# Kernel tuning notes

Measured on AMD Instinct MI355X. Metric: run time of the kernel, lower is better.

## Reference

```python
import jax, jax.numpy as jnp
import numpy as np
import math

C, NH, HD, L, P, FFN = 256, 8, 32, 1, 4, 512
H_BEV, W_BEV = 200, 100
NQ, BS, NV = 1000, 4, H_BEV * W_BEV
EPS = 1e-5


def _ln(x, g, b):
    m = x.mean(-1, keepdims=True)
    v = ((x - m) ** 2).mean(-1, keepdims=True)
    return (x - m) / jnp.sqrt(v + EPS) * g + b


def _mha(x, qpos, in_w, in_b, ow, ob):
    # nn.MultiheadAttention self-attention; key_pos = query_pos (shapes match)
    q = x + qpos
    k = x + qpos
    v = x
    wq, wk, wv = jnp.split(in_w, 3, axis=0)
    bq, bk, bv = jnp.split(in_b, 3, axis=0)
    bs, nq, _ = x.shape
    qh = (q @ wq.T + bq).reshape(bs, nq, NH, HD)
    kh = (k @ wk.T + bk).reshape(bs, nq, NH, HD)
    vh = (v @ wv.T + bv).reshape(bs, nq, NH, HD)
    scores = jnp.einsum('bqhd,bkhd->bhqk', qh, kh) / jnp.sqrt(jnp.float32(HD))
    attn = jax.nn.softmax(scores, axis=-1)
    out = jnp.einsum('bhqk,bkhd->bqhd', attn, vh).reshape(bs, nq, C)
    return out @ ow.T + ob


def _msdeform(x, qpos, value, ref, spatial_shapes, so_w, so_b, aw_w, aw_b, vp_w, vp_b, op_w, op_b):
    # Multi-scale deformable attention (single level), bilinear sampling with
    # align_corners=False convention and zero padding, as in the CUDA kernel.
    bs, nq, _ = x.shape
    q = x + qpos
    v = (value @ vp_w.T + vp_b).reshape(bs, NV, NH, HD).transpose(0, 2, 1, 3)  # [bs,nh,nv,hd]
    off = (q @ so_w.T + so_b).reshape(bs, nq, NH, L, P, 2)
    aw = jax.nn.softmax((q @ aw_w.T + aw_b).reshape(bs, nq, NH, L * P), axis=-1)
    aw = aw.reshape(bs, nq, NH, L, P)
    norm = jnp.stack([spatial_shapes[:, 1], spatial_shapes[:, 0]], -1).astype(jnp.float32)  # [L,2] = (W,H)
    loc = ref[:, :, None, :, None, :] + off / norm[None, None, None, :, None, :]  # [bs,nq,nh,L,P,2]
    loc = loc[:, :, :, 0]  # single level -> [bs,nq,nh,P,2]
    awp = aw[:, :, :, 0]   # [bs,nq,nh,P]
    x_im = loc[..., 0] * W_BEV - 0.5
    y_im = loc[..., 1] * H_BEV - 0.5
    x0 = jnp.floor(x_im)
    y0 = jnp.floor(y_im)
    lx = x_im - x0
    ly = y_im - y0
    x0i = x0.astype(jnp.int32)
    y0i = y0.astype(jnp.int32)
    acc = jnp.zeros((bs, NH, nq, P, HD), jnp.float32)
    for dy in (0, 1):
        for dx in (0, 1):
            xi = x0i + dx
            yi = y0i + dy
            w = (lx if dx else 1.0 - lx) * (ly if dy else 1.0 - ly)  # [bs,nq,nh,P]
            ok = ((xi >= 0) & (xi < W_BEV) & (yi >= 0) & (yi < H_BEV)).astype(jnp.float32)
            idx = jnp.clip(yi, 0, H_BEV - 1) * W_BEV + jnp.clip(xi, 0, W_BEV - 1)
            idx_t = idx.transpose(0, 2, 1, 3).reshape(bs, NH, nq * P)
            g = jnp.take_along_axis(v, idx_t[..., None], axis=2).reshape(bs, NH, nq, P, HD)
            acc = acc + g * (w * ok).transpose(0, 2, 1, 3)[..., None]
    out = (acc * awp.transpose(0, 2, 1, 3)[..., None]).sum(3)  # [bs,nh,nq,hd]
    out = out.transpose(0, 2, 1, 3).reshape(bs, nq, C)
    return out @ op_w.T + op_b


def setup_inputs() -> dict:
    key = jax.random.key(0)
    ks = jax.random.split(key, 24)
    f32 = jnp.float32

    def w(k, shp):
        fan = shp[-1]
        return (jax.random.normal(k, shp, f32) * (1.0 / np.sqrt(fan))).astype(f32)

    # sampling_offsets bias per _reset_parameters (radial grid init)
    thetas = np.arange(NH, dtype=np.float32) * (2.0 * math.pi / NH)
    grid = np.stack([np.cos(thetas), np.sin(thetas)], -1)
    grid = grid / np.abs(grid).max(-1, keepdims=True)
    grid = np.tile(grid[:, None, None, :], (1, L, P, 1))
    for i in range(P):
        grid[:, :, i, :] *= i + 1
    so_b = jnp.asarray(grid.reshape(-1), f32)

    return {
        'query': jax.random.normal(ks[0], (NQ, BS, C), f32),
        'value': jax.random.normal(ks[1], (NV, BS, C), f32),
        'query_pos': jax.random.normal(ks[2], (NQ, BS, C), f32),
        'reference_points': jax.random.uniform(ks[3], (BS, NQ, L, 2), f32),
        'spatial_shapes': jnp.array([[H_BEV, W_BEV]], jnp.int32),
        'level_start_index': jnp.zeros((L,), jnp.int32),
        'in_proj_w': w(ks[4], (3 * C, C)),
        'in_proj_b': jnp.zeros((3 * C,), f32),
        'mha_ow': w(ks[5], (C, C)),
        'mha_ob': jnp.zeros((C,), f32),
        'so_w': w(ks[6], (NH * L * P * 2, C)) * 0.01,
        'so_b': so_b,
        'aw_w': w(ks[7], (NH * L * P, C)) * 0.01,
        'aw_b': jnp.zeros((NH * L * P,), f32),
        'vp_w': w(ks[8], (C, C)),
        'vp_b': jnp.zeros((C,), f32),
        'op_w': w(ks[9], (C, C)),
        'op_b': jnp.zeros((C,), f32),
        'ffn_w1': w(ks[10], (FFN, C)),
        'ffn_b1': jnp.zeros((FFN,), f32),
        'ffn_w2': w(ks[11], (C, FFN)),
        'ffn_b2': jnp.zeros((C,), f32),
        'ln1_g': jnp.ones((C,), f32), 'ln1_b': jnp.zeros((C,), f32),
        'ln2_g': jnp.ones((C,), f32), 'ln2_b': jnp.zeros((C,), f32),
        'ln3_g': jnp.ones((C,), f32), 'ln3_b': jnp.zeros((C,), f32),
    }


def reference(query, value, query_pos, reference_points, spatial_shapes, level_start_index,
              in_proj_w, in_proj_b, mha_ow, mha_ob, so_w, so_b, aw_w, aw_b,
              vp_w, vp_b, op_w, op_b, ffn_w1, ffn_b1, ffn_w2, ffn_b2,
              ln1_g, ln1_b, ln2_g, ln2_b, ln3_g, ln3_b):
    # batch_first=False: (seq, bs, C) -> (bs, seq, C)
    x = query.transpose(1, 0, 2)
    val = value.transpose(1, 0, 2)
    qpos = query_pos.transpose(1, 0, 2)
    # self_attn -> norm (residual inside attn wrapper; dropout=0 in eval)
    x = _ln(x + _mha(x, qpos, in_proj_w, in_proj_b, mha_ow, mha_ob), ln1_g, ln1_b)
    # cross_attn (MSDeformAttn) -> norm
    x = _ln(x + _msdeform(x, qpos, val, reference_points, spatial_shapes,
                          so_w, so_b, aw_w, aw_b, vp_w, vp_b, op_w, op_b), ln2_g, ln2_b)
    # ffn -> norm
    h = jax.nn.relu(x @ ffn_w1.T + ffn_b1) @ ffn_w2.T + ffn_b2
    x = _ln(x + h, ln3_g, ln3_b)
    return x.transpose(1, 0, 2)
```

## Files before the change

### kernel.cpp

```cpp
#include <hip/hip_runtime.h>
#include <hip/hip_bf16.h>
#include <cmath>

#define BS   4
#define NQ   1000
#define CDIM 256
#define NH   8
#define HD   32
#define NVAL 20000
#define FFND 512
#define PN   4
#define WBEV 100
#define HBEV 200
#define TK   64

typedef __bf16 v8bf __attribute__((ext_vector_type(8)));
typedef float  v4f  __attribute__((ext_vector_type(4)));

__device__ __forceinline__ void gload_lds16(const void* g, void* l) {
    __builtin_amdgcn_global_load_lds(
        (const __attribute__((address_space(1))) unsigned int*)g,
        (__attribute__((address_space(3))) unsigned int*)l, 16, 0, 0);
}

__device__ __forceinline__ void vgemm64_block(
    int vb, const float* __restrict__ value, const __bf16* __restrict__ Wv,
    const float* __restrict__ bv, __bf16* __restrict__ vpj, char* smem)
{
    __bf16* As = (__bf16*)smem;
    __bf16* Bs = (__bf16*)(smem + 8192);
    int tid = threadIdx.x;
    int wave = tid >> 6, lane = tid & 63, quad = lane >> 4, n16 = lane & 15;
    int bm = vb * 64;
    int wm = (wave & 1) * 32, wn = (wave >> 1) * 128;
    v4f acc[2][8] = {};

    for (int k0 = 0; k0 < 256; k0 += 64) {
        float4 fa[2][2];
        #pragma unroll
        for (int i = 0; i < 2; i++) {
            int e = i * 256 + tid;
            int r = e >> 3, c = (e & 7) ^ (r & 7);
            const float* p = value + (long)(bm + r) * 256 + k0 + c * 8;
            fa[i][0] = *(const float4*)p;
            fa[i][1] = *(const float4*)(p + 4);
        }
        __syncthreads();
        #pragma unroll
        for (int i = 0; i < 2; i++) {
            int e = i * 256 + tid;
            v8bf v;
            v[0] = (__bf16)fa[i][0].x; v[1] = (__bf16)fa[i][0].y;
            v[2] = (__bf16)fa[i][0].z; v[3] = (__bf16)fa[i][0].w;
            v[4] = (__bf16)fa[i][1].x; v[5] = (__bf16)fa[i][1].y;
            v[6] = (__bf16)fa[i][1].z; v[7] = (__bf16)fa[i][1].w;
            *(v8bf*)(As + e * 8) = v;
        }
        #pragma unroll
        for (int i = 0; i < 8; i++) {
            int e = i * 256 + tid;
            int r = e >> 3, c = (e & 7) ^ (r & 7);
            gload_lds16(Wv + (long)r * 256 + k0 + c * 8, Bs + e * 8);
        }
        __syncthreads();
        #pragma unroll
        for (int s = 0; s < 2; s++) {
            v8bf af[2], bfr[8];
            #pragma unroll
            for (int mi = 0; mi < 2; mi++) {
                int row = wm + mi * 16 + n16;
                af[mi] = *(v8bf*)&As[row * 64 + (((quad + s * 4) ^ (row & 7))) * 8];
            }
            #pragma unroll
            for (int nj = 0; nj < 8; nj++) {
                int row = wn + nj * 16 + n16;
                bfr[nj] = *(v8bf*)&Bs[row * 64 + (((quad + s * 4) ^ (row & 7))) * 8];
            }
            #pragma unroll
            for (int mi = 0; mi < 2; mi++)
                #pragma unroll
                for (int nj = 0; nj < 8; nj++)
                    acc[mi][nj] = __builtin_amdgcn_mfma_f32_16x16x32_bf16(af[mi], bfr[nj], acc[mi][nj], 0, 0, 0);
        }
    }
    #pragma unroll
    for (int mi = 0; mi < 2; mi++) {
        #pragma unroll
        for (int r = 0; r < 4; r++) {
            int m = bm + wm + mi * 16 + quad * 4 + r;
            #pragma unroll
            for (int nj = 0; nj < 8; nj++) {
                int nn = wn + nj * 16 + n16;
                vpj[(long)m * 256 + nn] = (__bf16)(acc[mi][nj][r] + bv[nn]);
            }
        }
    }
}

__global__ __launch_bounds__(256) void prep_all_kernel(
    const float* __restrict__ query, const float* __restrict__ qpos,
    const float* __restrict__ in_w, const float* __restrict__ mha_ow,
    const float* __restrict__ vp_w, const float* __restrict__ op_w,
    const float* __restrict__ ffn_w1, const float* __restrict__ ffn_w2,
    const float* __restrict__ so_w, const float* __restrict__ aw_w,
    const float* __restrict__ so_b, const float* __restrict__ aw_b,
    float* __restrict__ x, float* __restrict__ qpos_t,
    __bf16* __restrict__ x_bf, __bf16* __restrict__ xq_bf,
    __bf16* __restrict__ wb, __bf16* __restrict__ wsmall,
    float* __restrict__ bsmall)
{
    int blk = blockIdx.x, tid = threadIdx.x;
    if (blk < 640) {
        long e = ((long)blk * 256 + tid) * 4;
        const float* src; long off;
        if      (e < 196608) { src = in_w;   off = e; }
        else if (e < 262144) { src = mha_ow; off = e - 196608; }
        else if (e < 327680) { src = vp_w;   off = e - 262144; }
        else if (e < 393216) { src = op_w;   off = e - 327680; }
        else if (e < 524288) { src = ffn_w1; off = e - 393216; }
        else                 { src = ffn_w2; off = e - 524288; }
        float4 v = *(const float4*)(src + off);
        __bf16* d = wb + e;
        d[0] = (__bf16)v.x; d[1] = (__bf16)v.y; d[2] = (__bf16)v.z; d[3] = (__bf16)v.w;
    } else if (blk < 4640) {
        int qb = blk - 640;
        int q = qb / BS, b = qb % BS;
        float qv = query[(q * BS + b) * CDIM + tid];
        float pv = qpos [(q * BS + b) * CDIM + tid];
        int o = (b * NQ + q) * CDIM + tid;
        x[o] = qv; qpos_t[o] = pv;
        x_bf[o] = (__bf16)qv; xq_bf[o] = (__bf16)(qv + pv);
    } else if (blk < 4672) {
        long e = ((long)(blk - 4640) * 256 + tid) * 4;
        int row = (int)(e >> 8), col = (int)(e & 255);
        float4 v = {0.f, 0.f, 0.f, 0.f};
        if (row < 64)      v = *(const float4*)(so_w + row * 256 + col);
        else if (row < 96) v = *(const float4*)(aw_w + (row - 64) * 256 + col);
        __bf16* d = wsmall + e;
        d[0] = (__bf16)v.x; d[1] = (__bf16)v.y; d[2] = (__bf16)v.z; d[3] = (__bf16)v.w;
    } else {
        if (tid < 128) bsmall[tid] = tid < 64 ? so_b[tid] : (tid < 96 ? aw_b[tid - 64] : 0.f);
    }
}

__global__ __launch_bounds__(256) void qkvv_kernel(
    const __bf16* __restrict__ xq, const __bf16* __restrict__ xv,
    const __bf16* __restrict__ W, const float* __restrict__ bias,
    __bf16* __restrict__ qk, __bf16* __restrict__ vh,
    const float* __restrict__ value, const __bf16* __restrict__ Wv,
    const float* __restrict__ bv, __bf16* __restrict__ vpj, int voff)
{
    __shared__ __align__(16) char smem[40960];
    int tid = threadIdx.x;
    if ((int)blockIdx.x >= 756) {
        vgemm64_block(blockIdx.x - 756 + voff, value, Wv, bv, vpj, smem);
        return;
    }
    int blk = blockIdx.x;
    int bn = (blk % 12) * 64, bm = (blk / 12) * 64;
    __bf16* As = (__bf16*)smem;
    __bf16* Bs = (__bf16*)(smem + 8192);
    const __bf16* A = (bn < 512) ? xq : xv;
    int wave = tid >> 6, lane = tid & 63, quad = lane >> 4, n16 = lane & 15;
    int wm = (wave & 1) * 32, wn = (wave >> 1) * 32;
    v4f acc[2][2] = {};

    for (int k0 = 0; k0 < 256; k0 += 64) {
        __syncthreads();
        #pragma unroll
        for (int i = 0; i < 2; i++) {
            int e = i * 256 + tid;
            int r = e >> 3, c = (e & 7) ^ (r & 7);
            int row = bm + r; if (row > BS * NQ - 1) row = BS * NQ - 1;
            gload_lds16(A + (long)row * 256 + k0 + c * 8, As + e * 8);
        }
        #pragma unroll
        for (int i = 0; i < 2; i++) {
            int e = i * 256 + tid;
            int r = e >> 3, c = (e & 7) ^ (r & 7);
            gload_lds16(W + (long)(bn + r) * 256 + k0 + c * 8, Bs + e * 8);
        }
        __syncthreads();
        #pragma unroll
        for (int s = 0; s < 2; s++) {
            v8bf af[2], bfr[2];
            #pragma unroll
            for (int mi = 0; mi < 2; mi++) {
                int row = wm + mi * 16 + n16;
                af[mi] = *(v8bf*)&As[row * 64 + (((quad + s * 4) ^ (row & 7))) * 8];
            }
            #pragma unroll
            for (int nj = 0; nj < 2; nj++) {
                int row = wn + nj * 16 + n16;
                bfr[nj] = *(v8bf*)&Bs[row * 64 + (((quad + s * 4) ^ (row & 7))) * 8];
            }
            #pragma unroll
            for (int mi = 0; mi < 2; mi++)
                #pragma unroll
                for (int nj = 0; nj < 2; nj++)
                    acc[mi][nj] = __builtin_amdgcn_mfma_f32_16x16x32_bf16(af[mi], bfr[nj], acc[mi][nj], 0, 0, 0);
        }
    }

    #pragma unroll
    for (int mi = 0; mi < 2; mi++) {
        #pragma unroll
        for (int r = 0; r < 4; r++) {
            int m = bm + wm + mi * 16 + quad * 4 + r;
            if (m >= BS * NQ) continue;
            #pragma unroll
            for (int nj = 0; nj < 2; nj++) {
                int nn = bn + wn + nj * 16 + n16;
                float v = acc[mi][nj][r] + bias[nn];
                if (nn < 512) qk[(long)m * 512 + nn] = (__bf16)v;
                else          vh[(long)m * 256 + (nn - 512)] = (__bf16)v;
            }
        }
    }
}

__global__ __launch_bounds__(256) void fattnv_kernel(
    const __bf16* __restrict__ qk, const __bf16* __restrict__ vh,
    __bf16* __restrict__ aout,
    const float* __restrict__ value, const __bf16* __restrict__ Wv,
    const float* __restrict__ bv, __bf16* __restrict__ vpj, int voff)
{
    __shared__ __align__(16) char smem[40960];
    int tid = threadIdx.x;
    if ((int)blockIdx.x >= 512) {
        vgemm64_block(blockIdx.x - 512 + voff, value, Wv, bv, vpj, smem);
        return;
    }
    int fb = blockIdx.x;
    int qt = fb & 15, h = (fb >> 4) & 7, b = fb >> 7;
    __bf16* Ks = (__bf16*)smem;
    __bf16* Vt = (__bf16*)(smem + 10240);
    __bf16* Pl = (__bf16*)(smem + 19456);
    int wave = tid >> 6, lane = tid & 63, quad = lane >> 4, n = lane & 15;
    int q0 = qt * 64 + wave * 16;
    const float scale = 0.17677669529663687f;
    const float M0 = 8.0f;

    int qrow = q0 + n; if (qrow > NQ - 1) qrow = NQ - 1;
    v8bf aq = *(const v8bf*)(qk + (long)(b * NQ + qrow) * 512 + h * HD + quad * 8);

    v4f o0 = {}, o1 = {};
    float lp[4] = {0.f, 0.f, 0.f, 0.f};

    int sv = tid >> 7;
    int t2 = tid & 127;
    int key = t2 & 63;
    int d16 = (t2 >> 6) * 16;

    v8bf stg0, stg1;
    auto loadtile = [&](int k0) {
        int krow = k0 + key; if (krow > NQ - 1) krow = NQ - 1;
        const __bf16* p = sv ? (vh + (long)(b * NQ + krow) * CDIM + h * HD + d16)
                             : (qk + (long)(b * NQ + krow) * 512 + 256 + h * HD + d16);
        stg0 = *(const v8bf*)p;
        stg1 = *(const v8bf*)(p + 8);
    };

    loadtile(0);
    int pb = 0;
    for (int k0 = 0; k0 < NQ; k0 += TK) {
        if (sv == 0) {
            *(v8bf*)&Ks[(pb * 64 + key) * 40 + d16]     = stg0;
            *(v8bf*)&Ks[(pb * 64 + key) * 40 + d16 + 8] = stg1;
        } else {
            #pragma unroll
            for (int j = 0; j < 8; j++) {
                Vt[(pb * 32 + d16 + j) * 72 + key]            = stg0[j];
                Vt[(pb * 32 + d16 + 8 + j) * 72 + (key ^ 16)] = stg1[j];
            }
        }
        if (k0 + TK < NQ) loadtile(k0 + TK);
        __syncthreads();

        v8bf bk0 = *(v8bf*)&Ks[(pb * 64 +      n) * 40 + quad * 8];
        v8bf bk1 = *(v8bf*)&Ks[(pb * 64 + 16 + n) * 40 + quad * 8];
        v8bf bk2 = *(v8bf*)&Ks[(pb * 64 + 32 + n) * 40 + quad * 8];
        v8bf bk3 = *(v8bf*)&Ks[(pb * 64 + 48 + n) * 40 + quad * 8];
        v4f z = {};
        v4f S0 = __builtin_amdgcn_mfma_f32_16x16x32_bf16(aq, bk0, z, 0, 0, 0);
        v4f S1 = __builtin_amdgcn_mfma_f32_16x16x32_bf16(aq, bk1, z, 0, 0, 0);
        v4f S2 = __builtin_amdgcn_mfma_f32_16x16x32_bf16(aq, bk2, z, 0, 0, 0);
        v4f S3 = __builtin_amdgcn_mfma_f32_16x16x32_bf16(aq, bk3, z, 0, 0, 0);

        bool last = (k0 + TK > NQ);
        float p0[4], p1[4], p2[4], p3[4];
        #pragma unroll
        for (int r = 0; r < 4; r++) {
            p0[r] = __expf(fmaf(S0[r], scale, -M0));
            p1[r] = __expf(fmaf(S1[r], scale, -M0));
            p2[r] = __expf(fmaf(S2[r], scale, -M0));
            p3[r] = __expf(fmaf(S3[r], scale, -M0));
            if (last) {
                if (k0 + 32 + n >= NQ) p2[r] = 0.f;
                if (k0 + 48 + n >= NQ) p3[r] = 0.f;
            }
            lp[r] += p0[r] + p1[r] + p2[r] + p3[r];
        }
        #pragma unroll
        for (int r = 0; r < 4; r++) {
            __bf16* pp = &Pl[(wave * 16 + quad * 4 + r) * 72];
            pp[n]      = (__bf16)p0[r];
            pp[16 + n] = (__bf16)p1[r];
            pp[32 + n] = (__bf16)p2[r];
            pp[48 + n] = (__bf16)p3[r];
        }
        asm volatile("s_waitcnt lgkmcnt(0)" ::: "memory");
        v8bf ap0 = *(v8bf*)&Pl[(wave * 16 + n) * 72 + quad * 8];
        v8bf ap1 = *(v8bf*)&Pl[(wave * 16 + n) * 72 + 32 + quad * 8];
        int swz = ((n >> 3) & 1) << 4;
        int c0 = (quad * 8) ^ swz;
        int c1 = (32 + quad * 8) ^ swz;
        v8bf bv00 = *(v8bf*)&Vt[(pb * 32 +      n) * 72 + c0];
        v8bf bv01 = *(v8bf*)&Vt[(pb * 32 +      n) * 72 + c1];
        v8bf bv10 = *(v8bf*)&Vt[(pb * 32 + 16 + n) * 72 + c0];
        v8bf bv11 = *(v8bf*)&Vt[(pb * 32 + 16 + n) * 72 + c1];
        o0 = __builtin_amdgcn_mfma_f32_16x16x32_bf16(ap0, bv00, o0, 0, 0, 0);
        o0 = __builtin_amdgcn_mfma_f32_16x16x32_bf16(ap1, bv01, o0, 0, 0, 0);
        o1 = __builtin_amdgcn_mfma_f32_16x16x32_bf16(ap0, bv10, o1, 0, 0, 0);
        o1 = __builtin_amdgcn_mfma_f32_16x16x32_bf16(ap1, bv11, o1, 0, 0, 0);
        pb ^= 1;
    }

    #pragma unroll
    for (int r = 0; r < 4; r++) {
        float l = lp[r];
        #pragma unroll
        for (int off = 1; off < 16; off <<= 1) l += __shfl_xor(l, off, 16);
        int q = q0 + quad * 4 + r;
        if (q < NQ) {
            float invl = 1.0f / l;
            __bf16* op = aout + ((long)(b * NQ + q) * CDIM + h * HD);
            op[n]      = (__bf16)(o0[r] * invl);
            op[16 + n] = (__bf16)(o1[r] * invl);
        }
    }
}

__global__ __launch_bounds__(256) void gln1s_kernel(
    const __bf16* __restrict__ A, const __bf16* __restrict__ W,
    const float* __restrict__ bias, const float* __restrict__ res,
    const float* __restrict__ g, const float* __restrict__ beta,
    const float* __restrict__ qpos_t,
    const __bf16* __restrict__ Wsm, const float* __restrict__ bsm,
    float* __restrict__ outf, float* __restrict__ soawO,
    const float* __restrict__ value, const __bf16* __restrict__ Wv,
    const float* __restrict__ bv, __bf16* __restrict__ vpj, int voff)
{
    __shared__ __align__(16) char smem[43776];
    int tid = threadIdx.x;
    if ((int)blockIdx.x >= 250) {
        vgemm64_block(blockIdx.x - 250 + voff, value, Wv, bv, vpj, smem);
        return;
    }
    __bf16* As  = (__bf16*)smem;
    __bf16* Bs  = (__bf16*)(smem + 2048);
    __bf16* Axq = (__bf16*)(smem + 34816);
    float* redS = (float*)(smem + 43264);
    float* redQ = redS + 64;
    int bm = blockIdx.x * 16;
    int wave = tid >> 6, lane = tid & 63, quad = lane >> 4, n16 = lane & 15;
    int wn = wave * 64;
    v4f acc[4] = {};

    for (int k0 = 0; k0 < 256; k0 += 64) {
        __syncthreads();
        if (tid < 128) {
            int e = tid;
            int r = e >> 3, c = (e & 7) ^ (r & 7);
            gload_lds16(A + (long)(bm + r) * 256 + k0 + c * 8, As + e * 8);
        }
        #pragma unroll
        for (int i = 0; i < 8; i++) {
            int e = i * 256 + tid;
            int r = e >> 3, c = (e & 7) ^ (r & 7);
            gload_lds16(W + (long)r * 256 + k0 + c * 8, Bs + e * 8);
        }
        __syncthreads();
        #pragma unroll
        for (int s = 0; s < 2; s++) {
            v8bf af = *(v8bf*)&As[n16 * 64 + (((quad + s * 4) ^ (n16 & 7))) * 8];
            #pragma unroll
            for (int nj = 0; nj < 4; nj++) {
                int row = wn + nj * 16 + n16;
                v8bf bfr = *(v8bf*)&Bs[row * 64 + (((quad + s * 4) ^ (row & 7))) * 8];
                acc[nj] = __builtin_amdgcn_mfma_f32_16x16x32_bf16(af, bfr, acc[nj], 0, 0, 0);
            }
        }
    }

    float y[4][4], s1[4] = {}, s2[4] = {};
    #pragma unroll
    for (int r = 0; r < 4; r++) {
        int m = bm + quad * 4 + r;
        #pragma unroll
        for (int nj = 0; nj < 4; nj++) {
            int nn = wn + nj * 16 + n16;
            float v = acc[nj][r] + bias[nn] + res[(long)m * 256 + nn];
            y[r][nj] = v;
            s1[r] += v; s2[r] += v * v;
        }
    }
    #pragma unroll
    for (int r = 0; r < 4; r++) {
        #pragma unroll
        for (int off = 1; off < 16; off <<= 1) {
            s1[r] += __shfl_xor(s1[r], off, 16);
            s2[r] += __shfl_xor(s2[r], off, 16);
        }
    }
    if (n16 == 0) {
        #pragma unroll
        for (int r = 0; r < 4; r++) {
            redS[wave * 16 + quad * 4 + r] = s1[r];
            redQ[wave * 16 + quad * 4 + r] = s2[r];
        }
    }
    __syncthreads();
    #pragma unroll
    for (int r = 0; r < 4; r++) {
        int mr = quad * 4 + r;
        float ts = redS[mr] + redS[16 + mr] + redS[32 + mr] + redS[48 + mr];
        float tq = redQ[mr] + redQ[16 + mr] + redQ[32 + mr] + redQ[48 + mr];
        float mean = ts * (1.0f / 256.0f);
        float var = tq * (1.0f / 256.0f) - mean * mean;
        float rinv = rsqrtf(var + 1e-5f);
        int m = bm + mr;
        #pragma unroll
        for (int nj = 0; nj < 4; nj++) {
            int nn = wn + nj * 16 + n16;
            float o = (y[r][nj] - mean) * rinv * g[nn] + beta[nn];
            outf[(long)m * 256 + nn] = o;
            Axq[mr * 264 + nn] = (__bf16)(o + qpos_t[(long)m * 256 + nn]);
        }
    }
    __syncthreads();
    if (wave < 3) {
        v4f sacc[2] = {};
        #pragma unroll
        for (int k0 = 0; k0 < 256; k0 += 32) {
            v8bf af = *(v8bf*)&Axq[n16 * 264 + k0 + quad * 8];
            #pragma unroll
            for (int t = 0; t < 2; t++) {
                int col = wave * 32 + t * 16 + n16;
                v8bf bw = *(const v8bf*)(Wsm + (long)col * 256 + k0 + quad * 8);
                sacc[t] = __builtin_amdgcn_mfma_f32_16x16x32_bf16(af, bw, sacc[t], 0, 0, 0);
            }
        }
        #pragma unroll
        for (int t = 0; t < 2; t++)
            #pragma unroll
            for (int r = 0; r < 4; r++) {
                int mm = bm + quad * 4 + r;
                int col = wave * 32 + t * 16 + n16;
                soawO[(long)mm * 96 + col] = sacc[t][r] + bsm[col];
            }
    }
}

__global__ __launch_bounds__(256) void msds_kernel(
    const __bf16* __restrict__ vproj, const float* __restrict__ soaw,
    const float* __restrict__ refp, __bf16* __restrict__ out)
{
    int bq = blockIdx.x; int b = bq / NQ; int q = bq % NQ;
    int t = threadIdx.x; int h = t / HD; int d = t % HD;
    float rx = refp[(b * NQ + q) * 2 + 0];
    float ry = refp[(b * NQ + q) * 2 + 1];
    const float* rowp = soaw + (long)(b * NQ + q) * 96;
    const float* offp = rowp + h * 8;
    const float* awp  = rowp + 64 + h * 4;
    float a0 = awp[0], a1 = awp[1], a2 = awp[2], a3 = awp[3];
    float m = fmaxf(fmaxf(a0, a1), fmaxf(a2, a3));
    float e0 = __expf(a0 - m), e1 = __expf(a1 - m), e2 = __expf(a2 - m), e3 = __expf(a3 - m);
    float invs = 1.0f / (e0 + e1 + e2 + e3);
    float acc = 0.f;
    #pragma unroll
    for (int p = 0; p < PN; p++) {
        float ew = (p == 0 ? e0 : p == 1 ? e1 : p == 2 ? e2 : e3) * invs;
        float xim = rx * (float)WBEV + offp[p * 2 + 0] - 0.5f;
        float yim = ry * (float)HBEV + offp[p * 2 + 1] - 0.5f;
        float x0f = floorf(xim), y0f = floorf(yim);
        float lx = xim - x0f, ly = yim - y0f;
        int x0 = (int)x0f, y0 = (int)y0f;
        float gsum = 0.f;
        #pragma unroll
        for (int dy = 0; dy < 2; dy++) {
            #pragma unroll
            for (int dx = 0; dx < 2; dx++) {
                int xi = x0 + dx, yi = y0 + dy;
                float w = (dx ? lx : 1.f - lx) * (dy ? ly : 1.f - ly);
                bool ok = (xi >= 0 && xi < WBEV && yi >= 0 && yi < HBEV);
                int xc = min(max(xi, 0), WBEV - 1);
                int yc = min(max(yi, 0), HBEV - 1);
                int idx = yc * WBEV + xc;
                float gv = (float)vproj[((long)(idx * BS + b)) * CDIM + h * HD + d];
                gsum += (ok ? w : 0.f) * gv;
            }
        }
        acc += ew * gsum;
    }
    out[(b * NQ + q) * CDIM + h * HD + d] = (__bf16)acc;
}

__global__ __launch_bounds__(256) void gln2_kernel(
    const __bf16* __restrict__ A, const __bf16* __restrict__ W,
    const float* __restrict__ bias, const float* __restrict__ res,
    const float* __restrict__ g, const float* __restrict__ beta,
    float* __restrict__ outf, __bf16* __restrict__ outb)
{
    __shared__ __align__(16) char smem[35328];
    __bf16* As = (__bf16*)smem;
    __bf16* Bs = (__bf16*)(smem + 2048);
    float* redS = (float*)(smem + 34816);
    float* redQ = redS + 64;
    int tid = threadIdx.x;
    int bm = blockIdx.x * 16;
    int wave = tid >> 6, lane = tid & 63, quad = lane >> 4, n16 = lane & 15;
    int wn = wave * 64;
    v4f acc[4] = {};

    for (int k0 = 0; k0 < 256; k0 += 64) {
        __syncthreads();
        if (tid < 128) {
            int e = tid;
            int r = e >> 3, c = (e & 7) ^ (r & 7);
            gload_lds16(A + (long)(bm + r) * 256 + k0 + c * 8, As + e * 8);
        }
        #pragma unroll
        for (int i = 0; i < 8; i++) {
            int e = i * 256 + tid;
            int r = e >> 3, c = (e & 7) ^ (r & 7);
            gload_lds16(W + (long)r * 256 + k0 + c * 8, Bs + e * 8);
        }
        __syncthreads();
        #pragma unroll
        for (int s = 0; s < 2; s++) {
            v8bf af = *(v8bf*)&As[n16 * 64 + (((quad + s * 4) ^ (n16 & 7))) * 8];
            #pragma unroll
            for (int nj = 0; nj < 4; nj++) {
                int row = wn + nj * 16 + n16;
                v8bf bfr = *(v8bf*)&Bs[row * 64 + (((quad + s * 4) ^ (row & 7))) * 8];
                acc[nj] = __builtin_amdgcn_mfma_f32_16x16x32_bf16(af, bfr, acc[nj], 0, 0, 0);
            }
        }
    }

    float y[4][4], s1[4] = {}, s2[4] = {};
    #pragma unroll
    for (int r = 0; r < 4; r++) {
        int m = bm + quad * 4 + r;
        #pragma unroll
        for (int nj = 0; nj < 4; nj++) {
            int nn = wn + nj * 16 + n16;
            float v = acc[nj][r] + bias[nn] + res[(long)m * 256 + nn];
            y[r][nj] = v;
            s1[r] += v; s2[r] += v * v;
        }
    }
    #pragma unroll
    for (int r = 0; r < 4; r++) {
        #pragma unroll
        for (int off = 1; off < 16; off <<= 1) {
            s1[r] += __shfl_xor(s1[r], off, 16);
            s2[r] += __shfl_xor(s2[r], off, 16);
        }
    }
    if (n16 == 0) {
        #pragma unroll
        for (int r = 0; r < 4; r++) {
            redS[wave * 16 + quad * 4 + r] = s1[r];
            redQ[wave * 16 + quad * 4 + r] = s2[r];
        }
    }
    __syncthreads();
    #pragma unroll
    for (int r = 0; r < 4; r++) {
        int mr = quad * 4 + r;
        float ts = redS[mr] + redS[16 + mr] + redS[32 + mr] + redS[48 + mr];
        float tq = redQ[mr] + redQ[16 + mr] + redQ[32 + mr] + redQ[48 + mr];
        float mean = ts * (1.0f / 256.0f);
        float var = tq * (1.0f / 256.0f) - mean * mean;
        float rinv = rsqrtf(var + 1e-5f);
        int m = bm + mr;
        #pragma unroll
        for (int nj = 0; nj < 4; nj++) {
            int nn = wn + nj * 16 + n16;
            float o = (y[r][nj] - mean) * rinv * g[nn] + beta[nn];
            outf[(long)m * 256 + nn] = o;
            outb[(long)m * 256 + nn] = (__bf16)o;
        }
    }
}

template<int TBM, int TBN>
__global__ __launch_bounds__(256) void mgemm_kernel(
    const __bf16* __restrict__ A, const __bf16* __restrict__ W,
    const float* __restrict__ bias, __bf16* __restrict__ Yb,
    int M, int N, int K, int relu, int nx)
{
    constexpr int SZ = TBM * 128 + TBN * 128;
    __shared__ __align__(16) char smem[SZ];
    constexpr int WMF = TBM / 32;
    constexpr int WNF = TBN / 32;
    __bf16* As = (__bf16*)smem;
    __bf16* Bs = (__bf16*)(smem + TBM * 128);
    int bm = (blockIdx.x / nx) * TBM, bn = (blockIdx.x % nx) * TBN;
    int tid = threadIdx.x;
    int wave = tid >> 6, lane = tid & 63, quad = lane >> 4, n16 = lane & 15;
    int wm = (wave & 1) * (TBM / 2), wn = (wave >> 1) * (TBN / 2);
    v4f acc[WMF][WNF] = {};

    for (int k0 = 0; k0 < K; k0 += 64) {
        __syncthreads();
        #pragma unroll
        for (int i = 0; i < TBM * 8 / 256; i++) {
            int e = i * 256 + tid;
            int r = e >> 3, c = (e & 7) ^ (r & 7);
            int row = bm + r; if (row > M - 1) row = M - 1;
            gload_lds16(A + (long)row * K + k0 + c * 8, As + e * 8);
        }
        #pragma unroll
        for (int i = 0; i < TBN * 8 / 256; i++) {
            int e = i * 256 + tid;
            int r = e >> 3, c = (e & 7) ^ (r & 7);
            gload_lds16(W + (long)(bn + r) * K + k0 + c * 8, Bs + e * 8);
        }
        __syncthreads();
        #pragma unroll
        for (int s = 0; s < 2; s++) {
            v8bf af[WMF], bfr[WNF];
            #pragma unroll
            for (int mi = 0; mi < WMF; mi++) {
                int row = wm + mi * 16 + n16;
                af[mi] = *(v8bf*)&As[row * 64 + (((quad + s * 4) ^ (row & 7))) * 8];
            }
            #pragma unroll
            for (int nj = 0; nj < WNF; nj++) {
                int row = wn + nj * 16 + n16;
                bfr[nj] = *(v8bf*)&Bs[row * 64 + (((quad + s * 4) ^ (row & 7))) * 8];
            }
            #pragma unroll
            for (int mi = 0; mi < WMF; mi++)
                #pragma unroll
                for (int nj = 0; nj < WNF; nj++)
                    acc[mi][nj] = __builtin_amdgcn_mfma_f32_16x16x32_bf16(af[mi], bfr[nj], acc[mi][nj], 0, 0, 0);
        }
    }

    #pragma unroll
    for (int mi = 0; mi < WMF; mi++) {
        #pragma unroll
        for (int r = 0; r < 4; r++) {
            int m = bm + wm + mi * 16 + quad * 4 + r;
            if (m >= M) continue;
            #pragma unroll
            for (int nj = 0; nj < WNF; nj++) {
                int nn = bn + wn + nj * 16 + n16;
                if (nn >= N) continue;
                float v = acc[mi][nj][r] + bias[nn];
                if (relu) v = fmaxf(v, 0.f);
                Yb[(long)m * N + nn] = (__bf16)v;
            }
        }
    }
}

__global__ __launch_bounds__(256) void gln3_kernel(
    const __bf16* __restrict__ A, const __bf16* __restrict__ W,
    const float* __restrict__ bias, const float* __restrict__ res,
    const float* __restrict__ g, const float* __restrict__ beta,
    float* __restrict__ outf)
{
    __shared__ __align__(16) char smem[35328];
    __bf16* As = (__bf16*)smem;
    __bf16* Bs = (__bf16*)(smem + 2048);
    float* redS = (float*)(smem + 34816);
    float* redQ = redS + 64;
    int tid = threadIdx.x;
    int bm = blockIdx.x * 16;
    int wave = tid >> 6, lane = tid & 63, quad = lane >> 4, n16 = lane & 15;
    int wn = wave * 64;
    v4f acc[4] = {};

    for (int k0 = 0; k0 < 512; k0 += 64) {
        __syncthreads();
        if (tid < 128) {
            int e = tid;
            int r = e >> 3, c = (e & 7) ^ (r & 7);
            gload_lds16(A + (long)(bm + r) * 512 + k0 + c * 8, As + e * 8);
        }
        #pragma unroll
        for (int i = 0; i < 8; i++) {
            int e = i * 256 + tid;
            int r = e >> 3, c = (e & 7) ^ (r & 7);
            gload_lds16(W + (long)r * 512 + k0 + c * 8, Bs + e * 8);
        }
        __syncthreads();
        #pragma unroll
        for (int s = 0; s < 2; s++) {
            v8bf af = *(v8bf*)&As[n16 * 64 + (((quad + s * 4) ^ (n16 & 7))) * 8];
            #pragma unroll
            for (int nj = 0; nj < 4; nj++) {
                int row = wn + nj * 16 + n16;
                v8bf bfr = *(v8bf*)&Bs[row * 64 + (((quad + s * 4) ^ (row & 7))) * 8];
                acc[nj] = __builtin_amdgcn_mfma_f32_16x16x32_bf16(af, bfr, acc[nj], 0, 0, 0);
            }
        }
    }

    float y[4][4], s1[4] = {}, s2[4] = {};
    #pragma unroll
    for (int r = 0; r < 4; r++) {
        int m = bm + quad * 4 + r;
        #pragma unroll
        for (int nj = 0; nj < 4; nj++) {
            int nn = wn + nj * 16 + n16;
            float v = acc[nj][r] + bias[nn] + res[(long)m * 256 + nn];
            y[r][nj] = v;
            s1[r] += v; s2[r] += v * v;
        }
    }
    #pragma unroll
    for (int r = 0; r < 4; r++) {
        #pragma unroll
        for (int off = 1; off < 16; off <<= 1) {
            s1[r] += __shfl_xor(s1[r], off, 16);
            s2[r] += __shfl_xor(s2[r], off, 16);
        }
    }
    if (n16 == 0) {
        #pragma unroll
        for (int r = 0; r < 4; r++) {
            redS[wave * 16 + quad * 4 + r] = s1[r];
            redQ[wave * 16 + quad * 4 + r] = s2[r];
        }
    }
    __syncthreads();
    #pragma unroll
    for (int r = 0; r < 4; r++) {
        int mr = quad * 4 + r;
        float ts = redS[mr] + redS[16 + mr] + redS[32 + mr] + redS[48 + mr];
        float tq = redQ[mr] + redQ[16 + mr] + redQ[32 + mr] + redQ[48 + mr];
        float mean = ts * (1.0f / 256.0f);
        float var = tq * (1.0f / 256.0f) - mean * mean;
        float rinv = rsqrtf(var + 1e-5f);
        int m = bm + mr;
        int b = m / NQ, q = m - b * NQ;
        #pragma unroll
        for (int nj = 0; nj < 4; nj++) {
            int nn = wn + nj * 16 + n16;
            float o = (y[r][nj] - mean) * rinv * g[nn] + beta[nn];
            outf[(long)(q * BS + b) * 256 + nn] = o;
        }
    }
}

extern "C" void kernel_launch(void* const* d_in, const int* in_sizes, int n_in,
                              void* d_out, int out_size, void* d_ws, size_t ws_size,
                              hipStream_t stream) {
    const float* query = (const float*)d_in[0];
    const float* value = (const float*)d_in[1];
    const float* qpos  = (const float*)d_in[2];
    const float* refp  = (const float*)d_in[3];
    const float* in_w  = (const float*)d_in[6];
    const float* in_b  = (const float*)d_in[7];
    const float* mha_ow = (const float*)d_in[8];
    const float* mha_ob = (const float*)d_in[9];
    const float* so_w  = (const float*)d_in[10];
    const float* so_b  = (const float*)d_in[11];
    const float* aw_w  = (const float*)d_in[12];
    const float* aw_b  = (const float*)d_in[13];
    const float* vp_w  = (const float*)d_in[14];
    const float* vp_b  = (const float*)d_in[15];
    const float* op_w  = (const float*)d_in[16];
    const float* op_b  = (const float*)d_in[17];
    const float* ffn_w1 = (const float*)d_in[18];
    const float* ffn_b1 = (const float*)d_in[19];
    const float* ffn_w2 = (const float*)d_in[20];
    const float* ffn_b2 = (const float*)d_in[21];
    const float* ln1_g = (const float*)d_in[22];
    const float* ln1_b = (const float*)d_in[23];
    const float* ln2_g = (const float*)d_in[24];
    const float* ln2_b = (const float*)d_in[25];
    const float* ln3_g = (const float*)d_in[26];
    const float* ln3_b = (const float*)d_in[27];
    float* out = (float*)d_out;

    const long NTOK = (long)BS * NQ * CDIM;

    float* x      = (float*)d_ws;
    float* qpos_t = x + NTOK;
    float* x1     = qpos_t + NTOK;
    float* x2     = x1 + NTOK;
    float* soaw   = x2 + NTOK;
    float* bsmall = soaw + (long)BS * NQ * 96;
    __bf16* x_bf   = (__bf16*)(bsmall + 128);
    __bf16* xq_bf  = x_bf + NTOK;
    __bf16* qk_bf  = xq_bf + NTOK;
    __bf16* vh_bf  = qk_bf + 2 * NTOK;
    __bf16* aA_bf  = vh_bf + NTOK;
    __bf16* x2_bf  = aA_bf + NTOK;
    __bf16* h1_bf  = x2_bf + NTOK;
    __bf16* vpj_bf = h1_bf + 2 * NTOK;
    __bf16* wb     = vpj_bf + (long)BS * NVAL * CDIM;
    __bf16* inw_b  = wb;
    __bf16* mow_b  = wb + 196608;
    __bf16* vpw_b  = wb + 262144;
    __bf16* opw_b  = wb + 327680;
    __bf16* fw1_b  = wb + 393216;
    __bf16* fw2_b  = wb + 524288;
    __bf16* wsmall = wb + 655360;

    dim3 blk(256);

    prep_all_kernel<<<4673, blk, 0, stream>>>(
        query, qpos, in_w, mha_ow, vp_w, op_w, ffn_w1, ffn_w2,
        so_w, aw_w, so_b, aw_b,
        x, qpos_t, x_bf, xq_bf, wb, wsmall, bsmall);

    qkvv_kernel<<<1173, blk, 0, stream>>>(xq_bf, x_bf, inw_b, in_b, qk_bf, vh_bf,
                                          value, vpw_b, vp_b, vpj_bf, 0);

    fattnv_kernel<<<929, blk, 0, stream>>>(qk_bf, vh_bf, aA_bf,
                                           value, vpw_b, vp_b, vpj_bf, 417);

    gln1s_kernel<<<666, blk, 0, stream>>>(
        aA_bf, mow_b, mha_ob, x, ln1_g, ln1_b, qpos_t, wsmall, bsmall,
        x1, soaw, value, vpw_b, vp_b, vpj_bf, 834);

    msds_kernel<<<BS * NQ, blk, 0, stream>>>(vpj_bf, soaw, refp, aA_bf);

    gln2_kernel<<<250, blk, 0, stream>>>(
        aA_bf, opw_b, op_b, x1, ln2_g, ln2_b, x2, x2_bf);

    mgemm_kernel<64, 64><<<504, blk, 0, stream>>>(
        x2_bf, fw1_b, ffn_b1, h1_bf, BS * NQ, 512, 256, 1, 8);

    gln3_kernel<<<250, blk, 0, stream>>>(
        h1_bf, fw2_b, ffn_b2, x2, ln3_g, ln3_b, out);
}
```

Measured before the change: 274.9 us.

## Fuse output-proj/LN2, FFN and LN3 into one tail kernel; vectorize deformable sampling

Merges three kernels (out-proj with LN2, the FFN first GEMM, and the FFN second GEMM with LN3) into one per-16-row kernel. The LN2 output and the ReLU hidden activations stay in swizzled LDS, so the x2 and h1 intermediates are never written to or read from global memory. This removes two launches. The deformable sampling kernel now handles two queries per block and two channels per thread using bf16x2 loads. The cost is that the fused kernel runs only 250 blocks with larger LDS use, which lowers parallelism for the FFN GEMMs.

```diff
diff --git a/kernel.cpp b/kernel.cpp
--- a/kernel.cpp
+++ b/kernel.cpp
@@ -15,6 +15,7 @@
 #define TK   64
 
 typedef __bf16 v8bf __attribute__((ext_vector_type(8)));
+typedef __bf16 v2bf __attribute__((ext_vector_type(2)));
 typedef float  v4f  __attribute__((ext_vector_type(4)));
 
 __device__ __forceinline__ void gload_lds16(const void* g, void* l) {
@@ -466,8 +467,12 @@
     const __bf16* __restrict__ vproj, const float* __restrict__ soaw,
     const float* __restrict__ refp, __bf16* __restrict__ out)
 {
-    int bq = blockIdx.x; int b = bq / NQ; int q = bq % NQ;
-    int t = threadIdx.x; int h = t / HD; int d = t % HD;
+    int t = threadIdx.x;
+    int bq = blockIdx.x * 2 + (t >> 7);
+    int b = bq / NQ; int q = bq % NQ;
+    int t2 = t & 127;
+    int h = t2 >> 4;
+    int d0 = (t2 & 15) * 2;
     float rx = refp[(b * NQ + q) * 2 + 0];
     float ry = refp[(b * NQ + q) * 2 + 1];
     const float* rowp = soaw + (long)(b * NQ + q) * 96;
@@ -477,7 +482,7 @@
     float m = fmaxf(fmaxf(a0, a1), fmaxf(a2, a3));
     float e0 = __expf(a0 - m), e1 = __expf(a1 - m), e2 = __expf(a2 - m), e3 = __expf(a3 - m);
     float invs = 1.0f / (e0 + e1 + e2 + e3);
-    float acc = 0.f;
+    float accA = 0.f, accB = 0.f;
     #pragma unroll
     for (int p = 0; p < PN; p++) {
         float ew = (p == 0 ? e0 : p == 1 ? e1 : p == 2 ? e2 : e3) * invs;
@@ -486,7 +491,7 @@
         float x0f = floorf(xim), y0f = floorf(yim);
         float lx = xim - x0f, ly = yim - y0f;
         int x0 = (int)x0f, y0 = (int)y0f;
-        float gsum = 0.f;
+        float gA = 0.f, gB = 0.f;
         #pragma unroll
         for (int dy = 0; dy < 2; dy++) {
             #pragma unroll
@@ -497,32 +502,41 @@
                 int xc = min(max(xi, 0), WBEV - 1);
                 int yc = min(max(yi, 0), HBEV - 1);
                 int idx = yc * WBEV + xc;
-                float gv = (float)vproj[((long)(idx * BS + b)) * CDIM + h * HD + d];
-                gsum += (ok ? w : 0.f) * gv;
-            }
-        }
-        acc += ew * gsum;
-    }
-    out[(b * NQ + q) * CDIM + h * HD + d] = (__bf16)acc;
-}
-
-__global__ __launch_bounds__(256) void gln2_kernel(
-    const __bf16* __restrict__ A, const __bf16* __restrict__ W,
-    const float* __restrict__ bias, const float* __restrict__ res,
-    const float* __restrict__ g, const float* __restrict__ beta,
-    float* __restrict__ outf, __bf16* __restrict__ outb)
+                v2bf gv = *(const v2bf*)(vproj + ((long)(idx * BS + b)) * CDIM + h * HD + d0);
+                float wk = (ok ? w : 0.f);
+                gA += wk * (float)gv[0];
+                gB += wk * (float)gv[1];
+            }
+        }
+        accA += ew * gA;
+        accB += ew * gB;
+    }
+    v2bf o2; o2[0] = (__bf16)accA; o2[1] = (__bf16)accB;
+    *(v2bf*)(out + (long)(b * NQ + q) * CDIM + h * HD + d0) = o2;
+}
+
+__global__ __launch_bounds__(256) void gtail_kernel(
+    const __bf16* __restrict__ A, const __bf16* __restrict__ Wop,
+    const float* __restrict__ opb, const float* __restrict__ res,
+    const float* __restrict__ g2, const float* __restrict__ b2ln,
+    const __bf16* __restrict__ W1, const float* __restrict__ b1,
+    const __bf16* __restrict__ W2, const float* __restrict__ bff2,
+    const float* __restrict__ g3, const float* __restrict__ b3ln,
+    float* __restrict__ outf)
 {
-    __shared__ __align__(16) char smem[35328];
-    __bf16* As = (__bf16*)smem;
-    __bf16* Bs = (__bf16*)(smem + 2048);
-    float* redS = (float*)(smem + 34816);
-    float* redQ = redS + 64;
+    __shared__ __align__(16) char smem[59904];
+    __bf16* As  = (__bf16*)smem;
+    __bf16* Bs  = (__bf16*)(smem + 2048);
+    __bf16* As2 = (__bf16*)(smem + 34816);
+    __bf16* h1s = (__bf16*)(smem + 43008);
+    float* redS = (float*)(smem + 59392);
+    float* redQ = (float*)(smem + 59648);
     int tid = threadIdx.x;
     int bm = blockIdx.x * 16;
     int wave = tid >> 6, lane = tid & 63, quad = lane >> 4, n16 = lane & 15;
     int wn = wave * 64;
+
     v4f acc[4] = {};
-
     for (int k0 = 0; k0 < 256; k0 += 64) {
         __syncthreads();
         if (tid < 128) {
@@ -534,7 +548,7 @@
         for (int i = 0; i < 8; i++) {
             int e = i * 256 + tid;
             int r = e >> 3, c = (e & 7) ^ (r & 7);
-            gload_lds16(W + (long)r * 256 + k0 + c * 8, Bs + e * 8);
+            gload_lds16(Wop + (long)r * 256 + k0 + c * 8, Bs + e * 8);
         }
         __syncthreads();
         #pragma unroll
@@ -548,16 +562,15 @@
             }
         }
     }
-
-    float y[4][4], s1[4] = {}, s2[4] = {};
+    float yv[4][4], s1[4] = {}, s2[4] = {};
     #pragma unroll
     for (int r = 0; r < 4; r++) {
         int m = bm + quad * 4 + r;
         #pragma unroll
         for (int nj = 0; nj < 4; nj++) {
             int nn = wn + nj * 16 + n16;
-            float v = acc[nj][r] + bias[nn] + res[(long)m * 256 + nn];
-            y[r][nj] = v;
+            float v = acc[nj][r] + opb[nn] + res[(long)m * 256 + nn];
+            yv[r][nj] = v;
             s1[r] += v; s2[r] += v * v;
         }
     }
@@ -585,158 +598,101 @@
         float mean = ts * (1.0f / 256.0f);
         float var = tq * (1.0f / 256.0f) - mean * mean;
         float rinv = rsqrtf(var + 1e-5f);
-        int m = bm + mr;
         #pragma unroll
         for (int nj = 0; nj < 4; nj++) {
             int nn = wn + nj * 16 + n16;
-            float o = (y[r][nj] - mean) * rinv * g[nn] + beta[nn];
-            outf[(long)m * 256 + nn] = o;
-            outb[(long)m * 256 + nn] = (__bf16)o;
-        }
-    }
-}
-
-template<int TBM, int TBN>
-__global__ __launch_bounds__(256) void mgemm_kernel(
-    const __bf16* __restrict__ A, const __bf16* __restrict__ W,
-    const float* __restrict__ bias, __bf16* __restrict__ Yb,
-    int M, int N, int K, int relu, int nx)
-{
-    constexpr int SZ = TBM * 128 + TBN * 128;
-    __shared__ __align__(16) char smem[SZ];
-    constexpr int WMF = TBM / 32;
-    constexpr int WNF = TBN / 32;
-    __bf16* As = (__bf16*)smem;
-    __bf16* Bs = (__bf16*)(smem + TBM * 128);
-    int bm = (blockIdx.x / nx) * TBM, bn = (blockIdx.x % nx) * TBN;
-    int tid = threadIdx.x;
-    int wave = tid >> 6, lane = tid & 63, quad = lane >> 4, n16 = lane & 15;
-    int wm = (wave & 1) * (TBM / 2), wn = (wave >> 1) * (TBN / 2);
-    v4f acc[WMF][WNF] = {};
-
-    for (int k0 = 0; k0 < K; k0 += 64) {
-        __syncthreads();
-        #pragma unroll
-        for (int i = 0; i < TBM * 8 / 256; i++) {
-            int e = i * 256 + tid;
-            int r = e >> 3, c = (e & 7) ^ (r & 7);
-            int row = bm + r; if (row > M - 1) row = M - 1;
-            gload_lds16(A + (long)row * K + k0 + c * 8, As + e * 8);
-        }
-        #pragma unroll
-        for (int i = 0; i < TBN * 8 / 256; i++) {
-            int e = i * 256 + tid;
-            int r = e >> 3, c = (e & 7) ^ (r & 7);
-            gload_lds16(W + (long)(bn + r) * K + k0 + c * 8, Bs + e * 8);
-        }
-        __syncthreads();
-        #pragma unroll
-        for (int s = 0; s < 2; s++) {
-            v8bf af[WMF], bfr[WNF];
-            #pragma unroll
-            for (int mi = 0; mi < WMF; mi++) {
-                int row = wm + mi * 16 + n16;
-                af[mi] = *(v8bf*)&As[row * 64 + (((quad + s * 4) ^ (row & 7))) * 8];
-            }
-            #pragma unroll
-            for (int nj = 0; nj < WNF; nj++) {
-                int row = wn + nj * 16 + n16;
-                bfr[nj] = *(v8bf*)&Bs[row * 64 + (((quad + s * 4) ^ (row & 7))) * 8];
-            }
-            #pragma unroll
-            for (int mi = 0; mi < WMF; mi++)
+            float o = (yv[r][nj] - mean) * rinv * g2[nn] + b2ln[nn];
+            yv[r][nj] = o;
+            int c = nn & 63;
+            As2[wave * 1024 + mr * 64 + ((((c >> 3)) ^ (mr & 7)) << 3) + (c & 7)] = (__bf16)o;
+        }
+    }
+
+    #pragma unroll 1
+    for (int H = 0; H < 2; H++) {
+        v4f accB[4] = {};
+        for (int k0 = 0; k0 < 256; k0 += 64) {
+            __syncthreads();
+            #pragma unroll
+            for (int i = 0; i < 8; i++) {
+                int e = i * 256 + tid;
+                int r = e >> 3, c = (e & 7) ^ (r & 7);
+                gload_lds16(W1 + (long)(H * 256 + r) * 256 + k0 + c * 8, Bs + e * 8);
+            }
+            __syncthreads();
+            int kc = k0 >> 6;
+            #pragma unroll
+            for (int s = 0; s < 2; s++) {
+                v8bf af = *(v8bf*)&As2[kc * 1024 + n16 * 64 + (((quad + s * 4) ^ (n16 & 7))) * 8];
                 #pragma unroll
-                for (int nj = 0; nj < WNF; nj++)
-                    acc[mi][nj] = __builtin_amdgcn_mfma_f32_16x16x32_bf16(af[mi], bfr[nj], acc[mi][nj], 0, 0, 0);
-        }
-    }
-
-    #pragma unroll
-    for (int mi = 0; mi < WMF; mi++) {
+                for (int nj = 0; nj < 4; nj++) {
+                    int row = wn + nj * 16 + n16;
+                    v8bf bfr = *(v8bf*)&Bs[row * 64 + (((quad + s * 4) ^ (row & 7))) * 8];
+                    accB[nj] = __builtin_amdgcn_mfma_f32_16x16x32_bf16(af, bfr, accB[nj], 0, 0, 0);
+                }
+            }
+        }
         #pragma unroll
         for (int r = 0; r < 4; r++) {
-            int m = bm + wm + mi * 16 + quad * 4 + r;
-            if (m >= M) continue;
-            #pragma unroll
-            for (int nj = 0; nj < WNF; nj++) {
-                int nn = bn + wn + nj * 16 + n16;
-                if (nn >= N) continue;
-                float v = acc[mi][nj][r] + bias[nn];
-                if (relu) v = fmaxf(v, 0.f);
-                Yb[(long)m * N + nn] = (__bf16)v;
-            }
-        }
-    }
-}
-
-__global__ __launch_bounds__(256) void gln3_kernel(
-    const __bf16* __restrict__ A, const __bf16* __restrict__ W,
-    const float* __restrict__ bias, const float* __restrict__ res,
-    const float* __restrict__ g, const float* __restrict__ beta,
-    float* __restrict__ outf)
-{
-    __shared__ __align__(16) char smem[35328];
-    __bf16* As = (__bf16*)smem;
-    __bf16* Bs = (__bf16*)(smem + 2048);
-    float* redS = (float*)(smem + 34816);
-    float* redQ = redS + 64;
-    int tid = threadIdx.x;
-    int bm = blockIdx.x * 16;
-    int wave = tid >> 6, lane = tid & 63, quad = lane >> 4, n16 = lane & 15;
-    int wn = wave * 64;
-    v4f acc[4] = {};
-
+            int mr = quad * 4 + r;
+            #pragma unroll
+            for (int nj = 0; nj < 4; nj++) {
+                int col = H * 256 + wn + nj * 16 + n16;
+                float v = accB[nj][r] + b1[col];
+                v = fmaxf(v, 0.f);
+                int kc = col >> 6, c = col & 63;
+                h1s[kc * 1024 + mr * 64 + ((((c >> 3)) ^ (mr & 7)) << 3) + (c & 7)] = (__bf16)v;
+            }
+        }
+    }
+
+    v4f acc3[4] = {};
     for (int k0 = 0; k0 < 512; k0 += 64) {
         __syncthreads();
-        if (tid < 128) {
-            int e = tid;
-            int r = e >> 3, c = (e & 7) ^ (r & 7);
-            gload_lds16(A + (long)(bm + r) * 512 + k0 + c * 8, As + e * 8);
-        }
         #pragma unroll
         for (int i = 0; i < 8; i++) {
             int e = i * 256 + tid;
             int r = e >> 3, c = (e & 7) ^ (r & 7);
-            gload_lds16(W + (long)r * 512 + k0 + c * 8, Bs + e * 8);
-        }
-        __syncthreads();
+            gload_lds16(W2 + (long)r * 512 + k0 + c * 8, Bs + e * 8);
+        }
+        __syncthreads();
+        int kc = k0 >> 6;
         #pragma unroll
         for (int s = 0; s < 2; s++) {
-            v8bf af = *(v8bf*)&As[n16 * 64 + (((quad + s * 4) ^ (n16 & 7))) * 8];
+            v8bf af = *(v8bf*)&h1s[kc * 1024 + n16 * 64 + (((quad + s * 4) ^ (n16 & 7))) * 8];
             #pragma unroll
             for (int nj = 0; nj < 4; nj++) {
                 int row = wn + nj * 16 + n16;
                 v8bf bfr = *(v8bf*)&Bs[row * 64 + (((quad + s * 4) ^ (row & 7))) * 8];
-                acc[nj] = __builtin_amdgcn_mfma_f32_16x16x32_bf16(af, bfr, acc[nj], 0, 0, 0);
-            }
-        }
-    }
-
-    float y[4][4], s1[4] = {}, s2[4] = {};
-    #pragma unroll
-    for (int r = 0; r < 4; r++) {
-        int m = bm + quad * 4 + r;
+                acc3[nj] = __builtin_amdgcn_mfma_f32_16x16x32_bf16(af, bfr, acc3[nj], 0, 0, 0);
+            }
+        }
+    }
+    float y3[4][4], t1[4] = {}, t2[4] = {};
+    #pragma unroll
+    for (int r = 0; r < 4; r++) {
         #pragma unroll
         for (int nj = 0; nj < 4; nj++) {
             int nn = wn + nj * 16 + n16;
-            float v = acc[nj][r] + bias[nn] + res[(long)m * 256 + nn];
-            y[r][nj] = v;
-            s1[r] += v; s2[r] += v * v;
+            float v = acc3[nj][r] + bff2[nn] + yv[r][nj];
+            y3[r][nj] = v;
+            t1[r] += v; t2[r] += v * v;
         }
     }
     #pragma unroll
     for (int r = 0; r < 4; r++) {
         #pragma unroll
         for (int off = 1; off < 16; off <<= 1) {
-            s1[r] += __shfl_xor(s1[r], off, 16);
-            s2[r] += __shfl_xor(s2[r], off, 16);
-        }
-    }
+            t1[r] += __shfl_xor(t1[r], off, 16);
+            t2[r] += __shfl_xor(t2[r], off, 16);
+        }
+    }
+    __syncthreads();
     if (n16 == 0) {
         #pragma unroll
         for (int r = 0; r < 4; r++) {
-            redS[wave * 16 + quad * 4 + r] = s1[r];
-            redQ[wave * 16 + quad * 4 + r] = s2[r];
+            redS[wave * 16 + quad * 4 + r] = t1[r];
+            redQ[wave * 16 + quad * 4 + r] = t2[r];
         }
     }
     __syncthreads();
@@ -753,7 +709,7 @@
         #pragma unroll
         for (int nj = 0; nj < 4; nj++) {
             int nn = wn + nj * 16 + n16;
-            float o = (y[r][nj] - mean) * rinv * g[nn] + beta[nn];
+            float o = (y3[r][nj] - mean) * rinv * g3[nn] + b3ln[nn];
             outf[(long)(q * BS + b) * 256 + nn] = o;
         }
     }
@@ -832,14 +788,9 @@
         aA_bf, mow_b, mha_ob, x, ln1_g, ln1_b, qpos_t, wsmall, bsmall,
         x1, soaw, value, vpw_b, vp_b, vpj_bf, 834);
 
-    msds_kernel<<<BS * NQ, blk, 0, stream>>>(vpj_bf, soaw, refp, aA_bf);
-
-    gln2_kernel<<<250, blk, 0, stream>>>(
-        aA_bf, opw_b, op_b, x1, ln2_g, ln2_b, x2, x2_bf);
-
-    mgemm_kernel<64, 64><<<504, blk, 0, stream>>>(
-        x2_bf, fw1_b, ffn_b1, h1_bf, BS * NQ, 512, 256, 1, 8);
-
-    gln3_kernel<<<250, blk, 0, stream>>>(
-        h1_bf, fw2_b, ffn_b2, x2, ln3_g, ln3_b, out);
-}
+    msds_kernel<<<2000, blk, 0, stream>>>(vpj_bf, soaw, refp, aA_bf);
+
+    gtail_kernel<<<250, blk, 0, stream>>>(
+        aA_bf, opw_b, op_b, x1, ln2_g, ln2_b,
+        fw1_b, ffn_b1, fw2_b, ffn_b2, ln3_g, ln3_b, out);
+}
```

Measured after the change: 270.5 us. Within noise of the previous version (-1.6%).
